# Kernel tuning notes

Measured on AMD Instinct MI355X. Metric: run time of the kernel, lower is better.

The kernel has to match this reference:

```python
import jax, jax.numpy as jnp
import numpy as np

B, N, E, H, F, L, S = 4, 384, 768, 32, 3072, 12, 512
D = E // H


def setup_inputs() -> dict:
    key = jax.random.key(0)
    ks = jax.random.split(key, 32)
    inp = {}
    # forward args
    inp['node_type'] = jax.random.randint(ks[0], (B, N, 1), 1, S + 1)  # table has S+1 rows; 0 = pad (unused)
    inp['node_input_feature'] = jax.random.normal(ks[1], (B, N, E), jnp.float32)
    inp['in_degree'] = jax.random.randint(ks[2], (B, N), 0, S)
    inp['out_degree'] = jax.random.randint(ks[3], (B, N), 0, S)
    inp['attn_bias'] = jax.random.normal(ks[4], (B, N, N), jnp.float32) * 0.1
    inp['spatial_pos'] = jax.random.randint(ks[5], (B, N, N), 0, S)
    # embedding tables (normal stddev 0.02, as in the flax module)
    inp['node_emb'] = jax.random.normal(ks[6], (S + 1, E), jnp.float32) * 0.02
    inp['in_deg_emb'] = jax.random.normal(ks[7], (S, E), jnp.float32) * 0.02
    inp['out_deg_emb'] = jax.random.normal(ks[8], (S, E), jnp.float32) * 0.02
    inp['sp_emb'] = jax.random.normal(ks[9], (S, H), jnp.float32) * 0.02
    inp['sp_emb_rev'] = jax.random.normal(ks[10], (S, H), jnp.float32) * 0.02
    # per-layer weights, stacked along leading L axis
    se, sf = 1.0 / np.sqrt(E), 1.0 / np.sqrt(F)
    inp['Wq'] = jax.random.normal(ks[11], (L, E, E), jnp.float32) * se
    inp['bq'] = jax.random.normal(ks[12], (L, E), jnp.float32) * se
    inp['Wk'] = jax.random.normal(ks[13], (L, E, E), jnp.float32) * se
    inp['bk'] = jax.random.normal(ks[14], (L, E), jnp.float32) * se
    inp['Wv'] = jax.random.normal(ks[15], (L, E, E), jnp.float32) * se
    inp['bv'] = jax.random.normal(ks[16], (L, E), jnp.float32) * se
    inp['Wo'] = jax.random.normal(ks[17], (L, E, E), jnp.float32) * se
    inp['bo'] = jnp.zeros((L, E), jnp.float32)
    inp['W1'] = jax.random.normal(ks[18], (L, E, F), jnp.float32) * se
    inp['b1'] = jax.random.normal(ks[19], (L, F), jnp.float32) * se
    inp['W2'] = jax.random.normal(ks[20], (L, F, E), jnp.float32) * sf
    inp['b2'] = jax.random.normal(ks[21], (L, E), jnp.float32) * sf
    inp['ln1_s'] = jnp.ones((L, E), jnp.float32)
    inp['ln1_b'] = jnp.zeros((L, E), jnp.float32)
    inp['ln2_s'] = jnp.ones((L, E), jnp.float32)
    inp['ln2_b'] = jnp.zeros((L, E), jnp.float32)
    return inp


def _layernorm(x, scale, bias, eps=1e-5):
    m = x.mean(-1, keepdims=True)
    v = ((x - m) ** 2).mean(-1, keepdims=True)
    return (x - m) / jnp.sqrt(v + eps) * scale + bias


def _encoder(node_type, node_input_feature, in_degree, out_degree, attn_bias, spatial_pos,
             node_emb, in_deg_emb, out_deg_emb, sp_emb, sp_emb_rev,
             Wq, bq, Wk, bk, Wv, bv, Wo, bo, W1, b1, W2, b2, ln1_s, ln1_b, ln2_s, ln2_b):
    nt = node_type[..., 0]                               # [B,N]
    padding_mask = nt == 0                               # [B,N]
    # node features: node_emb(node_type).sum(-2) + degree embeddings + input feature
    x = (node_emb[node_type].sum(axis=-2)
         + in_deg_emb[in_degree] + out_deg_emb[out_degree]
         + node_input_feature)                           # [B,N,E]
    # spatial attention bias: [B,N,N,H] -> [B,H,N,N], plus graph-level attn_bias
    sb = sp_emb[spatial_pos] + sp_emb_rev[jnp.transpose(spatial_pos, (0, 2, 1))]
    bias = jnp.transpose(sb, (0, 3, 1, 2)) + attn_bias[:, None]  # [B,H,N,N]

    x = jnp.transpose(x, (1, 0, 2))                      # [N,B,E]
    scaling = D ** (-0.5)
    neg_inf = jnp.float32(-jnp.inf)

    def layer(x, p):
        wq, bq_, wk, bk_, wv, bv_, wo, bo_, w1, b1_, w2, b2_, s1, t1, s2, t2 = p
        q = ((x @ wq) + bq_) * scaling                   # [N,B,E], bias scaled too (faithful)
        k = (x @ wk) + bk_
        v = (x @ wv) + bv_
        q = q.reshape(N, B, H, D)
        k = k.reshape(N, B, H, D)
        v = v.reshape(N, B, H, D)
        w = jnp.einsum('nbhd,mbhd->bhnm', q, k) + bias   # [B,H,N,N]
        w = jnp.where(padding_mask[:, None, None, :], neg_inf, w)
        probs = jax.nn.softmax(w.astype(jnp.float32), axis=-1).astype(x.dtype)
        a = jnp.einsum('bhnm,mbhd->nbhd', probs, v).reshape(N, B, E)
        a = a @ wo + bo_
        x = _layernorm(x + a, s1, t1)                    # post-LN
        h = jax.nn.gelu(x @ w1 + b1_)                    # approximate gelu (flax default)
        h = h @ w2 + b2_
        x = _layernorm(x + h, s2, t2)
        return x, None

    xs = (Wq, bq, Wk, bk, Wv, bv, Wo, bo, W1, b1, W2, b2, ln1_s, ln1_b, ln2_s, ln2_b)
    x, _ = jax.lax.scan(layer, x, xs)
    return x                                             # [N,B,E]


def reference(node_type, node_input_feature, in_degree, out_degree, attn_bias, spatial_pos,
              node_emb, in_deg_emb, out_deg_emb, sp_emb, sp_emb_rev,
              Wq, bq, Wk, bk, Wv, bv, Wo, bo, W1, b1, W2, b2, ln1_s, ln1_b, ln2_s, ln2_b):
    return _encoder(node_type, node_input_feature, in_degree, out_degree, attn_bias, spatial_pos,
                    node_emb, in_deg_emb, out_deg_emb, sp_emb, sp_emb_rev,
                    Wq, bq, Wk, bk, Wv, bv, Wo, bo, W1, b1, W2, b2, ln1_s, ln1_b, ln2_s, ln2_b)
```

## Files before the change

### kernel.cpp

```cpp
#include <hip/hip_runtime.h>
#include <hip/hip_bf16.h>

#define Bb 4
#define Nn 384
#define Ee 768
#define Hh 32
#define Ff 3072
#define Ll 12
#define Ss 512
#define Mm (Nn*Bb)

typedef __attribute__((ext_vector_type(8))) short bf16x8;
typedef __attribute__((ext_vector_type(4))) float f32x4;
typedef unsigned short u16;

__device__ __forceinline__ u16 f2b(float f) {
  union { float f; unsigned int i; } c; c.f = f;
  unsigned int x = c.i;
  return (u16)((x + 0x7fffu + ((x >> 16) & 1u)) >> 16);
}
__device__ __forceinline__ float b2f(u16 u) {
  union { unsigned int i; float f; } c; c.i = ((unsigned int)u) << 16; return c.f;
}
__device__ __forceinline__ unsigned pkcvt(float lo, float hi) {
  unsigned r;
  asm("v_cvt_pk_bf16_f32 %0, %1, %2" : "=v"(r) : "v"(lo), "v"(hi));
  return r;
}
__device__ __forceinline__ void gload_lds16(const void* g, void* l) {
  __builtin_amdgcn_global_load_lds((__attribute__((address_space(1))) void*)(g),
                                   (__attribute__((address_space(3))) void*)(l), 16, 0, 0);
}

__device__ __forceinline__ void embed_body(
    int r, const int* __restrict__ node_type, const float* __restrict__ nif,
    const int* __restrict__ in_deg, const int* __restrict__ out_deg,
    const float* __restrict__ node_emb, const float* __restrict__ ind_emb,
    const float* __restrict__ outd_emb,
    float* __restrict__ x, u16* __restrict__ xb)
{
  const int n = r / Bb, b = r % Bb;
  const int nt  = node_type[b*Nn + n];
  const int idg = in_deg[b*Nn + n];
  const int odg = out_deg[b*Nn + n];
  for (int c = threadIdx.x; c < Ee; c += 256) {
    float val = node_emb[(size_t)nt*Ee + c] + ind_emb[(size_t)idg*Ee + c]
              + outd_emb[(size_t)odg*Ee + c] + nif[((size_t)b*Nn + n)*Ee + c];
    x[(size_t)r*Ee + c] = val;
    xb[(size_t)r*Ee + c] = f2b(val);
  }
}

__device__ __forceinline__ void spT_body(
    int bid, char* smemRaw, const int* __restrict__ sp, int* __restrict__ spT)
{
  int (*tile)[33] = (int(*)[33])smemRaw;
  const int b = bid / 144, rem = bid % 144;
  const int m0 = (rem % 12) * 32, n0 = (rem / 12) * 32;
  const int tx = threadIdx.x & 31, ty = threadIdx.x >> 5;
  for (int i = ty; i < 32; i += 8)
    tile[i][tx] = sp[((size_t)b*Nn + n0 + i)*Nn + m0 + tx];
  __syncthreads();
  for (int i = ty; i < 32; i += 8)
    spT[((size_t)b*Nn + m0 + i)*Nn + n0 + tx] = tile[tx][i];
}

__device__ __forceinline__ void biaspre_body(
    int bid2, char* smemRaw,
    const float* __restrict__ atb, const int* __restrict__ sp, const int* __restrict__ spT,
    const float* __restrict__ sp_emb, const float* __restrict__ sp_emb_rev,
    u16* __restrict__ biasb)
{
  float* spc  = (float*)smemRaw;
  float* sprc = spc + 512;
  const int bx = bid2 % 24, h = (bid2 / 24) % Hh, b = bid2 / (24 * Hh);
  const int t = threadIdx.x;
  for (int i = t; i < 512; i += 256) {
    spc[i]  = sp_emb[(size_t)i*Hh + h];
    sprc[i] = sp_emb_rev[(size_t)i*Hh + h];
  }
  __syncthreads();
  const int qi = t >> 4;
  const int ml = (t & 15) << 2;
  const size_t rowb = ((size_t)b*Nn + bx*16 + qi)*Nn;
  u16* outb = biasb + ((size_t)(b*Hh + h)*24 + bx)*24*256;
  #pragma unroll
  for (int mg = 0; mg < 6; ++mg) {
    const int m = mg*64 + ml;
    float4 a4 = *(const float4*)(atb + rowb + m);
    int4  s4 = *(const int4*)(sp  + rowb + m);
    int4  t4 = *(const int4*)(spT + rowb + m);
    const int tt = m >> 4, hi2 = (m >> 2) & 3;
    uint2 u;
    u.x = pkcvt(a4.x + spc[s4.x] + sprc[t4.x], a4.y + spc[s4.y] + sprc[t4.y]);
    u.y = pkcvt(a4.z + spc[s4.z] + sprc[t4.z], a4.w + spc[s4.w] + sprc[t4.w]);
    *(uint2*)(outb + (tt >> 1)*512 + (hi2*16 + qi)*8 + (tt & 1)*4) = u;
  }
}

__device__ __forceinline__ void wconv_body(
    int tid, int layer, char* smemRaw,
    const float* Wq, const float* Wk, const float* Wv,
    const float* Wo, const float* W1, const float* W2, u16* slot)
{
  float (*tile)[65] = (float(*)[65])smemRaw;
  const float* src; u16* dst; int Ns, Ks;
  if (tid < 432)       { int seg = tid / 144; tid -= seg*144;
                         src = (seg==0?Wq:(seg==1?Wk:Wv)) + (size_t)layer*Ee*Ee;
                         dst = slot + (size_t)seg*589824; Ns = 768; Ks = 768; }
  else if (tid < 576)  { tid -= 432; src = Wo + (size_t)layer*Ee*Ee; dst = slot + 1769472; Ns = 768;  Ks = 768; }
  else if (tid < 1152) { tid -= 576; src = W1 + (size_t)layer*Ee*Ff; dst = slot + 2359296; Ns = 3072; Ks = 768; }
  else                 { tid -= 1152; src = W2 + (size_t)layer*Ff*Ee; dst = slot + 4718592; Ns = 768; Ks = 3072; }
  const int tc = Ns >> 6;
  const int tk = tid / tc, tn = tid % tc;
  const int t = threadIdx.x;
  #pragma unroll
  for (int i = 0; i < 4; ++i) {
    const int id = t + i*256;
    const int r = id >> 4, c = (id & 15) << 2;
    float4 v = *(const float4*)(src + (size_t)(tk*64 + r)*Ns + tn*64 + c);
    tile[r][c+0] = v.x; tile[r][c+1] = v.y; tile[r][c+2] = v.z; tile[r][c+3] = v.w;
  }
  __syncthreads();
  #pragma unroll
  for (int i = 0; i < 2; ++i) {
    const int ch = t + i*256;
    const int n = ch >> 3, kc = (ch & 7) << 3;
    uint4 u;
    u.x = pkcvt(tile[kc+0][n], tile[kc+1][n]);
    u.y = pkcvt(tile[kc+2][n], tile[kc+3][n]);
    u.z = pkcvt(tile[kc+4][n], tile[kc+5][n]);
    u.w = pkcvt(tile[kc+6][n], tile[kc+7][n]);
    *(uint4*)(dst + (size_t)(tn*64 + n)*Ks + tk*64 + kc) = u;
  }
}

__global__ __launch_bounds__(256) void wconv_kernel(
    const float* __restrict__ Wq, const float* __restrict__ Wk, const float* __restrict__ Wv,
    const float* __restrict__ Wo, const float* __restrict__ W1, const float* __restrict__ W2,
    int layer, u16* __restrict__ slot)
{
  __shared__ __align__(16) char smem[16640];
  wconv_body(blockIdx.x, layer, smem, Wq, Wk, Wv, Wo, W1, W2, slot);
}

__global__ __launch_bounds__(256) void prep_kernel(
    const int* __restrict__ node_type, const float* __restrict__ nif,
    const int* __restrict__ in_deg, const int* __restrict__ out_deg,
    const float* __restrict__ node_emb, const float* __restrict__ ind_emb,
    const float* __restrict__ outd_emb,
    float* __restrict__ x, u16* __restrict__ xb,
    const int* __restrict__ sp, int* __restrict__ spT,
    const float* __restrict__ Wq, const float* __restrict__ Wk, const float* __restrict__ Wv,
    const float* __restrict__ Wo, const float* __restrict__ W1, const float* __restrict__ W2,
    u16* __restrict__ slot0)
{
  __shared__ __align__(16) char smem[16640];
  const int bid = blockIdx.x;
  if (bid < 1536) {
    embed_body(bid, node_type, nif, in_deg, out_deg, node_emb, ind_emb, outd_emb, x, xb);
  } else if (bid < 2112) {
    spT_body(bid - 1536, smem, sp, spT);
  } else {
    wconv_body(bid - 2112, 0, smem, Wq, Wk, Wv, Wo, W1, W2, slot0);
  }
}

template<int EPI>
__device__ __forceinline__ void gemm_body(
    char* smemRaw, int bx0, int by0, int gx, int nwg, int zz,
    const u16* __restrict__ A, const u16* __restrict__ Bw,
    const float* __restrict__ b0, const float* __restrict__ b1, const float* __restrict__ b2,
    int Kfull, int Kc, float scaleQ,
    float* __restrict__ outF, u16* __restrict__ outB)
{
  u16 (*As)[128][64] = (u16(*)[128][64])smemRaw;
  u16 (*Bs)[64][64]  = (u16(*)[64][64])(smemRaw + 32768);
  const int t = threadIdx.x, lane = t & 63, wave = t >> 6;
  int bx = bx0, by = by0;
  {
    const int bid = bx + gx * by;
    const int cpx = nwg >> 3;
    const int s = (bid & 7) * cpx + (bid >> 3);
    bx = s % gx; by = s / gx;
  }
  const int m0 = bx * 128, n0 = by * 64;
  const int k0 = zz * Kc;
  const int wm = wave >> 1, wn = wave & 1;
  const int ql = lane & 15, hi = lane >> 4;
  const int nk = Kc >> 6;
  const int sr = t >> 3;
  const int sslot = (t & 7) ^ (sr & 7);
  const size_t aoff = (size_t)(m0 + sr)*Kfull + k0 + (sslot << 3);
  const size_t boff = (size_t)(n0 + sr)*Kfull + k0 + (sslot << 3);
  const size_t rstep = (size_t)32 * Kfull;

  int aro[4][2], bro[2][2];
  #pragma unroll
  for (int ks = 0; ks < 2; ++ks) {
    const int kb = (((ks<<2) + hi) ^ (ql & 7)) << 4;
    #pragma unroll
    for (int f = 0; f < 4; ++f) aro[f][ks] = (wm*64 + f*16 + ql)*128 + kb;
    #pragma unroll
    for (int f = 0; f < 2; ++f) bro[f][ks] = (wn*32 + f*16 + ql)*128 + kb;
  }

  f32x4 acc[4][2];
  #pragma unroll
  for (int a = 0; a < 4; ++a)
    #pragma unroll
    for (int c = 0; c < 2; ++c) acc[a][c] = (f32x4){0.f,0.f,0.f,0.f};

  #pragma unroll
  for (int i = 0; i < 4; ++i)
    gload_lds16(A + aoff + i*rstep, (char*)&As[0][0][0] + i*4096 + t*16);
  #pragma unroll
  for (int i = 0; i < 2; ++i)
    gload_lds16(Bw + boff + i*rstep, (char*)&Bs[0][0][0] + i*4096 + t*16);

  for (int kt = 0; kt < nk; ++kt) {
    const int cur = kt & 1, nxt = cur ^ 1;
    const bool pre = (kt + 1 < nk);
    if (pre) {
      const size_t kk = (size_t)(kt + 1) << 6;
      #pragma unroll
      for (int i = 0; i < 4; ++i)
        gload_lds16(A + aoff + kk + i*rstep, (char*)&As[nxt][0][0] + i*4096 + t*16);
      #pragma unroll
      for (int i = 0; i < 2; ++i)
        gload_lds16(Bw + boff + kk + i*rstep, (char*)&Bs[nxt][0][0] + i*4096 + t*16);
      asm volatile("s_waitcnt vmcnt(6)" ::: "memory");
    } else {
      asm volatile("s_waitcnt vmcnt(0)" ::: "memory");
    }
    __builtin_amdgcn_s_barrier();
    __builtin_amdgcn_sched_barrier(0);

    const char* aBase = (const char*)&As[cur][0][0];
    const char* bBase = (const char*)&Bs[cur][0][0];
    bf16x8 af[4][2], bf[2][2];
    #pragma unroll
    for (int f = 0; f < 4; ++f)
      #pragma unroll
      for (int ks = 0; ks < 2; ++ks)
        af[f][ks] = *(const bf16x8*)(aBase + aro[f][ks]);
    #pragma unroll
    for (int f = 0; f < 2; ++f)
      #pragma unroll
      for (int ks = 0; ks < 2; ++ks)
        bf[f][ks] = *(const bf16x8*)(bBase + bro[f][ks]);
    #pragma unroll
    for (int ks = 0; ks < 2; ++ks)
      #pragma unroll
      for (int fm = 0; fm < 4; ++fm)
        #pragma unroll
        for (int fn = 0; fn < 2; ++fn)
          acc[fm][fn] = __builtin_amdgcn_mfma_f32_16x16x32_bf16(af[fm][ks], bf[fn][ks], acc[fm][fn], 0, 0, 0);
    if (pre) {
      __builtin_amdgcn_sched_barrier(0);
      __builtin_amdgcn_s_barrier();
    }
  }

  #pragma unroll
  for (int fm = 0; fm < 4; ++fm) {
    const int rowb = m0 + wm*64 + fm*16 + hi*4;
    #pragma unroll
    for (int fn = 0; fn < 2; ++fn) {
      const int gcol = n0 + wn*32 + fn*16 + ql;
      float bv, scale = 1.0f;
      if (EPI == 0) {
        const int seg = gcol / 768;
        const int cw = gcol - seg*768;
        bv = (seg == 0) ? b0[cw] : ((seg == 1) ? b1[cw] : b2[cw]);
        if (seg == 0) scale = scaleQ;
      } else if (EPI == 1) {
        bv = (zz == 0) ? b0[gcol] : 0.0f;
      } else {
        bv = b0[gcol];
      }
      f32x4 v = acc[fm][fn];
      #pragma unroll
      for (int j = 0; j < 4; ++j) {
        float val = (v[j] + bv) * scale;
        if (EPI == 0) {
          outB[(size_t)(rowb + j) * 2304 + gcol] = f2b(val);
        } else if (EPI == 1) {
          outF[(size_t)zz * (Mm*768) + (size_t)(rowb + j) * 768 + gcol] = val;
        } else {
          float arg = 0.7978845608028654f * (val + 0.044715f * val * val * val);
          float e = __expf(2.0f * arg);
          float g = 0.5f * val * (2.0f - 2.0f / (e + 1.0f));
          outB[(size_t)(rowb + j) * 3072 + gcol] = f2b(g);
        }
      }
    }
  }
}

template<int EPI>
__global__ __launch_bounds__(256) void gemm3_kernel(
    const u16* __restrict__ A, const u16* __restrict__ Bw,
    const float* __restrict__ b0, const float* __restrict__ b1, const float* __restrict__ b2,
    int Kfull, int Kc, float scaleQ,
    float* __restrict__ outF, u16* __restrict__ outB)
{
  __shared__ __align__(16) char smem[49152];
  gemm_body<EPI>(smem, blockIdx.x, blockIdx.y, gridDim.x, gridDim.x*gridDim.y,
                 blockIdx.z, A, Bw, b0, b1, b2, Kfull, Kc, scaleQ, outF, outB);
}

__global__ __launch_bounds__(256) void qkv0b_kernel(
    const u16* __restrict__ A, const u16* __restrict__ qkvT,
    const float* __restrict__ b0, const float* __restrict__ b1, const float* __restrict__ b2,
    float scaleQ, u16* __restrict__ outB,
    const float* __restrict__ atb, const int* __restrict__ sp, const int* __restrict__ spT,
    const float* __restrict__ sp_emb, const float* __restrict__ sp_emb_rev,
    u16* __restrict__ biasb)
{
  __shared__ __align__(16) char smem[49152];
  const int bid = blockIdx.x;
  if (bid < 432) {
    gemm_body<0>(smem, bid % 12, bid / 12, 12, 432, 0,
                 A, qkvT, b0, b1, b2, 768, 768, scaleQ, nullptr, outB);
  } else {
    biaspre_body(bid - 432, smem, atb, sp, spT, sp_emb, sp_emb_rev, biasb);
  }
}

__global__ __launch_bounds__(256) void ffn2w_kernel(
    const u16* __restrict__ A, const u16* __restrict__ w2T,
    const float* __restrict__ b2v, float* __restrict__ outF,
    const float* __restrict__ Wq, const float* __restrict__ Wk, const float* __restrict__ Wv,
    const float* __restrict__ Wo, const float* __restrict__ W1, const float* __restrict__ W2,
    int layerNext, u16* __restrict__ slotNext, int doW)
{
  __shared__ __align__(16) char smem[49152];
  const int bid = blockIdx.x;
  if (bid < 576) {
    const int zz = bid / 144, r = bid - zz*144;
    gemm_body<1>(smem, r % 12, r / 12, 12, 144, zz,
                 A, w2T, b2v, b2v, b2v, 3072, 768, 1.0f, outF, nullptr);
  } else if (doW) {
    wconv_body(bid - 576, layerNext, smem, Wq, Wk, Wv, Wo, W1, W2, slotNext);
  }
}

template<int PREBIAS>
__global__ __launch_bounds__(256) void attn2_kernel(
    const u16* __restrict__ qkv,
    const u16* __restrict__ biasb,
    const float* __restrict__ atb, const int* __restrict__ sp, const int* __restrict__ spT,
    const float* __restrict__ sp_emb, const float* __restrict__ sp_emb_rev,
    u16* __restrict__ ab)
{
  __shared__ __align__(16) u16 Kt[384][32];
  __shared__ __align__(16) u16 Vt[32][392];
  __shared__ __align__(16) u16 Qt[128][32];
  __shared__ __align__(16) u16 Pw[4][16][32];
  __shared__ float spc[512], sprc[512];
  const int bid = blockIdx.x;
  const int pair = bid % 3;
  const int h = (bid / 3) % Hh;
  const int b = bid / (3 * Hh);
  const int t = threadIdx.x, lane = t & 63, wave = t >> 6;
  const int ql = lane & 15, hi = lane >> 4;

  for (int idx = t; idx < 384*3; idx += 256) {
    const int m = idx / 3, c = idx - m*3;
    const u16* base = qkv + ((size_t)m*Bb + b)*2304 + h*24 + c*8;
    uint4 kk = *(const uint4*)(base + 768);
    uint4 vv = *(const uint4*)(base + 1536);
    *(uint4*)&Kt[m][c*8] = kk;
    Vt[c*8+0][m] = (u16)(vv.x & 0xffffu); Vt[c*8+1][m] = (u16)(vv.x >> 16);
    Vt[c*8+2][m] = (u16)(vv.y & 0xffffu); Vt[c*8+3][m] = (u16)(vv.y >> 16);
    Vt[c*8+4][m] = (u16)(vv.z & 0xffffu); Vt[c*8+5][m] = (u16)(vv.z >> 16);
    Vt[c*8+6][m] = (u16)(vv.w & 0xffffu); Vt[c*8+7][m] = (u16)(vv.w >> 16);
  }
  for (int idx = t; idx < 384*2; idx += 256)
    *(uint2*)&Kt[idx>>1][24 + (idx&1)*4] = make_uint2(0u, 0u);
  for (int idx = t; idx < 8*196; idx += 256)
    *(unsigned*)((char*)&Vt[24][0] + idx*4) = 0u;
  for (int idx = t; idx < 128*3; idx += 256) {
    const int qr = idx / 3, c = idx - qr*3;
    const u16* base = qkv + ((size_t)(pair*128 + qr)*Bb + b)*2304 + h*24 + c*8;
    *(uint4*)&Qt[qr][c*8] = *(const uint4*)base;
  }
  for (int idx = t; idx < 128*2; idx += 256)
    *(uint2*)&Qt[idx>>1][24 + (idx&1)*4] = make_uint2(0u, 0u);
  if (!PREBIAS) {
    for (int i = t; i < 512; i += 256) {
      spc[i]  = sp_emb[(size_t)i*Hh + h];
      sprc[i] = sp_emb_rev[(size_t)i*Hh + h];
    }
  }
  __syncthreads();

  for (int qi = 0; qi < 2; ++qi) {
    const int ntile = pair*2 + qi;
    const int q0 = ntile*64 + wave*16;
    const int q = q0 + ql;
    const bf16x8 qf = *(const bf16x8*)&Qt[qi*64 + wave*16 + ql][hi*8];

    f32x4 f[24];
    const size_t crow = ((size_t)b*Nn + q)*Nn;
    if (PREBIAS) {
      const u16* bp = biasb + (((size_t)(b*Hh + h)*24 + ntile*4 + wave)*24)*256 + lane*8;
      #pragma unroll
      for (int tt2 = 0; tt2 < 12; ++tt2) {
        uint4 bb = *(const uint4*)(bp + tt2*512);
        {
          bf16x8 kf = *(const bf16x8*)&Kt[(2*tt2)*16 + ql][hi*8];
          f32x4 z = (f32x4){0.f,0.f,0.f,0.f};
          f32x4 s = __builtin_amdgcn_mfma_f32_16x16x32_bf16(kf, qf, z, 0, 0, 0);
          s[0] += b2f((u16)(bb.x & 0xffffu)); s[1] += b2f((u16)(bb.x >> 16));
          s[2] += b2f((u16)(bb.y & 0xffffu)); s[3] += b2f((u16)(bb.y >> 16));
          f[2*tt2] = s;
        }
        {
          bf16x8 kf = *(const bf16x8*)&Kt[(2*tt2+1)*16 + ql][hi*8];
          f32x4 z = (f32x4){0.f,0.f,0.f,0.f};
          f32x4 s = __builtin_amdgcn_mfma_f32_16x16x32_bf16(kf, qf, z, 0, 0, 0);
          s[0] += b2f((u16)(bb.z & 0xffffu)); s[1] += b2f((u16)(bb.z >> 16));
          s[2] += b2f((u16)(bb.w & 0xffffu)); s[3] += b2f((u16)(bb.w >> 16));
          f[2*tt2+1] = s;
        }
      }
    } else {
      #pragma unroll
      for (int tt = 0; tt < 24; ++tt) {
        bf16x8 kf = *(const bf16x8*)&Kt[tt*16 + ql][hi*8];
        f32x4 z = (f32x4){0.f,0.f,0.f,0.f};
        f32x4 s = __builtin_amdgcn_mfma_f32_16x16x32_bf16(kf, qf, z, 0, 0, 0);
        const int off = tt*16 + hi*4;
        int4 s4 = *(const int4*)(sp + crow + off);
        int4 t4 = *(const int4*)(spT + crow + off);
        float4 a4 = *(const float4*)(atb + crow + off);
        s[0] += a4.x + spc[s4.x] + sprc[t4.x];
        s[1] += a4.y + spc[s4.y] + sprc[t4.y];
        s[2] += a4.z + spc[s4.z] + sprc[t4.z];
        s[3] += a4.w + spc[s4.w] + sprc[t4.w];
        f[tt] = s;
      }
    }

    float mx = -3.0e38f;
    #pragma unroll
    for (int tt = 0; tt < 24; ++tt)
      mx = fmaxf(mx, fmaxf(fmaxf(f[tt][0], f[tt][1]), fmaxf(f[tt][2], f[tt][3])));
    mx = fmaxf(mx, __shfl_xor(mx, 16, 64));
    mx = fmaxf(mx, __shfl_xor(mx, 32, 64));
    float sum = 0.f;
    #pragma unroll
    for (int tt = 0; tt < 24; ++tt) {
      #pragma unroll
      for (int j = 0; j < 4; ++j) { f[tt][j] = __expf(f[tt][j] - mx); sum += f[tt][j]; }
    }
    sum += __shfl_xor(sum, 16, 64);
    sum += __shfl_xor(sum, 32, 64);
    const float inv = 1.0f / sum;

    f32x4 o0 = (f32x4){0.f,0.f,0.f,0.f}, o1 = (f32x4){0.f,0.f,0.f,0.f};
    char* prow = (char*)&Pw[wave][ql][0];
    const int swz = (ql & 3) << 4;
    #pragma unroll
    for (int c = 0; c < 12; ++c) {
      unsigned w0 = pkcvt(f[2*c][0],   f[2*c][1]);
      unsigned w1 = pkcvt(f[2*c][2],   f[2*c][3]);
      unsigned w2 = pkcvt(f[2*c+1][0], f[2*c+1][1]);
      unsigned w3 = pkcvt(f[2*c+1][2], f[2*c+1][3]);
      *(unsigned*)(prow + (((hi*8)      ) ^ swz)) = w0;
      *(unsigned*)(prow + (((hi*8) +  4) ^ swz)) = w1;
      *(unsigned*)(prow + (((hi*8) + 32) ^ swz)) = w2;
      *(unsigned*)(prow + (((hi*8) + 36) ^ swz)) = w3;
      bf16x8 a = *(const bf16x8*)(prow + ((hi*16) ^ swz));
      bf16x8 v0 = *(const bf16x8*)&Vt[ql][c*32 + hi*8];
      bf16x8 v1 = *(const bf16x8*)&Vt[16 + ql][c*32 + hi*8];
      o0 = __builtin_amdgcn_mfma_f32_16x16x32_bf16(a, v0, o0, 0, 0, 0);
      o1 = __builtin_amdgcn_mfma_f32_16x16x32_bf16(a, v1, o1, 0, 0, 0);
    }

    #pragma unroll
    for (int j = 0; j < 4; ++j) {
      float invj = __shfl(inv, hi*4 + j, 64);
      const int qg = q0 + hi*4 + j;
      u16* orow = ab + ((size_t)qg*Bb + b)*Ee + h*24;
      orow[ql] = f2b(o0[j] * invj);
      if (ql < 8) orow[16 + ql] = f2b(o1[j] * invj);
    }
  }
}

template<int NP>
__global__ __launch_bounds__(256) void ln_kernel(
    const float* __restrict__ xin, const float* __restrict__ delta,
    const float* __restrict__ gamma, const float* __restrict__ beta,
    float* __restrict__ xout, u16* __restrict__ xb)
{
  const int wave = threadIdx.x >> 6, lane = threadIdx.x & 63;
  const int r = blockIdx.x * 4 + wave;
  const size_t base = (size_t)r * Ee;
  const int c0 = lane * 12;
  float v[12];
  #pragma unroll
  for (int i = 0; i < 3; ++i) {
    float4 xv = *(const float4*)(xin + base + c0 + i*4);
    v[i*4+0] = xv.x; v[i*4+1] = xv.y; v[i*4+2] = xv.z; v[i*4+3] = xv.w;
  }
  #pragma unroll
  for (int p = 0; p < NP; ++p) {
    const float* dp = delta + (size_t)p*(Mm*768) + base + c0;
    #pragma unroll
    for (int i = 0; i < 3; ++i) {
      float4 dv = *(const float4*)(dp + i*4);
      v[i*4+0] += dv.x; v[i*4+1] += dv.y; v[i*4+2] += dv.z; v[i*4+3] += dv.w;
    }
  }
  float s = 0.f;
  #pragma unroll
  for (int i = 0; i < 12; ++i) s += v[i];
  #pragma unroll
  for (int off = 1; off < 64; off <<= 1) s += __shfl_xor(s, off, 64);
  const float mean = s * (1.0f / 768.0f);
  float qs = 0.f;
  #pragma unroll
  for (int i = 0; i < 12; ++i) { float d = v[i] - mean; qs += d * d; }
  #pragma unroll
  for (int off = 1; off < 64; off <<= 1) qs += __shfl_xor(qs, off, 64);
  const float rstd = rsqrtf(qs * (1.0f / 768.0f) + 1e-5f);
  float o[12];
  #pragma unroll
  for (int i = 0; i < 3; ++i) {
    float4 g4 = *(const float4*)(gamma + c0 + i*4);
    float4 b4 = *(const float4*)(beta + c0 + i*4);
    o[i*4+0] = (v[i*4+0] - mean) * rstd * g4.x + b4.x;
    o[i*4+1] = (v[i*4+1] - mean) * rstd * g4.y + b4.y;
    o[i*4+2] = (v[i*4+2] - mean) * rstd * g4.z + b4.z;
    o[i*4+3] = (v[i*4+3] - mean) * rstd * g4.w + b4.w;
    *(float4*)(xout + base + c0 + i*4) = make_float4(o[i*4+0], o[i*4+1], o[i*4+2], o[i*4+3]);
  }
  #pragma unroll
  for (int i = 0; i < 3; ++i) {
    uint2 u;
    u.x = pkcvt(o[i*4+0], o[i*4+1]);
    u.y = pkcvt(o[i*4+2], o[i*4+3]);
    *(uint2*)(xb + base + c0 + i*4) = u;
  }
}

extern "C" void kernel_launch(void* const* d_in, const int* in_sizes, int n_in,
                              void* d_out, int out_size, void* d_ws, size_t ws_size,
                              hipStream_t stream) {
  const int*   node_type  = (const int*)d_in[0];
  const float* nif        = (const float*)d_in[1];
  const int*   in_deg     = (const int*)d_in[2];
  const int*   out_deg    = (const int*)d_in[3];
  const float* atb        = (const float*)d_in[4];
  const int*   sp         = (const int*)d_in[5];
  const float* node_emb   = (const float*)d_in[6];
  const float* ind_emb    = (const float*)d_in[7];
  const float* outd_emb   = (const float*)d_in[8];
  const float* sp_emb     = (const float*)d_in[9];
  const float* sp_emb_rev = (const float*)d_in[10];
  const float* Wq = (const float*)d_in[11]; const float* bq = (const float*)d_in[12];
  const float* Wk = (const float*)d_in[13]; const float* bk = (const float*)d_in[14];
  const float* Wv = (const float*)d_in[15]; const float* bv = (const float*)d_in[16];
  const float* Wo = (const float*)d_in[17]; const float* bo = (const float*)d_in[18];
  const float* W1 = (const float*)d_in[19]; const float* b1 = (const float*)d_in[20];
  const float* W2 = (const float*)d_in[21]; const float* b2 = (const float*)d_in[22];
  const float* ln1s = (const float*)d_in[23]; const float* ln1b = (const float*)d_in[24];
  const float* ln2s = (const float*)d_in[25]; const float* ln2b = (const float*)d_in[26];

  char* ws = (char*)d_ws;
  float* x      = (float*)(ws);
  u16*   xb     = (u16*)(ws +  4718592);
  u16*   qkvb16 = (u16*)(ws +  7077888);
  u16*   abuf   = (u16*)(ws + 14155776);
  u16*   hb     = (u16*)(ws + 16515072);
  float* obufP  = (float*)(ws + 25952256);
  int*   spTb   = (int*)(ws + 44826624);
  u16*   biasb  = (u16*)(ws + 47185920);
  u16*   wTs0   = (u16*)(ws + 84934656);
  u16*   wTs1   = (u16*)(ws + 99090432);
  const bool useBias = ws_size >= 113246208ull;
  u16* slots[2] = { wTs0, wTs1 };

  prep_kernel<<<3840, 256, 0, stream>>>(node_type, nif, in_deg, out_deg,
                                        node_emb, ind_emb, outd_emb, x, xb,
                                        sp, spTb,
                                        Wq, Wk, Wv, Wo, W1, W2, slots[0]);

  const float scaleQ = 0.2041241452319315f;

  for (int l = 0; l < Ll; ++l) {
    const float *bql = bq + (size_t)l*Ee, *bkl = bk + (size_t)l*Ee, *bvl = bv + (size_t)l*Ee;
    const float *bol = bo + (size_t)l*Ee;
    const float *b1l = b1 + (size_t)l*Ff, *b2l = b2 + (size_t)l*Ee;

    u16* slot = slots[l & 1];
    u16* slotN = slots[(l + 1) & 1];
    const u16* qkvT = slot;
    const u16* woT  = slot + 1769472;
    const u16* w1T  = slot + 2359296;
    const u16* w2T  = slot + 4718592;

    if (l == 0 && useBias)
      qkv0b_kernel<<<3504, 256, 0, stream>>>(xb, qkvT, bql, bkl, bvl, scaleQ, qkvb16,
                                             atb, sp, spTb, sp_emb, sp_emb_rev, biasb);
    else
      gemm3_kernel<0><<<dim3(12, 36), 256, 0, stream>>>(xb, qkvT, bql, bkl, bvl,
                                                        768, 768, scaleQ, nullptr, qkvb16);
    if (useBias)
      attn2_kernel<1><<<384, 256, 0, stream>>>(qkvb16, biasb, atb, sp, spTb,
                                               sp_emb, sp_emb_rev, abuf);
    else
      attn2_kernel<0><<<384, 256, 0, stream>>>(qkvb16, nullptr, atb, sp, spTb,
                                               sp_emb, sp_emb_rev, abuf);
    gemm3_kernel<1><<<dim3(12, 12, 2), 256, 0, stream>>>(abuf, woT, bol, bol, bol,
                                                         768, 384, 1.0f, obufP, nullptr);
    ln_kernel<2><<<Mm/4, 256, 0, stream>>>(x, obufP, ln1s + (size_t)l*Ee, ln1b + (size_t)l*Ee, x, xb);
    gemm3_kernel<2><<<dim3(12, 48), 256, 0, stream>>>(xb, w1T, b1l, b1l, b1l,
                                                      768, 768, 1.0f, nullptr, hb);
    ffn2w_kernel<<<2304, 256, 0, stream>>>(hb, w2T, b2l, obufP,
                                           Wq, Wk, Wv, Wo, W1, W2,
                                           l + 1, slotN, (l + 1 < Ll) ? 1 : 0);
    float* xdst = (l == Ll - 1) ? (float*)d_out : x;
    ln_kernel<4><<<Mm/4, 256, 0, stream>>>(x, obufP, ln2s + (size_t)l*Ee, ln2b + (size_t)l*Ee, xdst, xb);
  }
}
```

Baseline: 1.174 ms.

## Fuse output-projection GEMM and LayerNorm into one launch with a global counter

Merges the Wo split-K GEMM and the following residual+LayerNorm into a single kernel. GEMM blocks increment a per-layer atomic counter after a threadfence, and LN blocks spin-wait until all 288 GEMM blocks finish. This removes one kernel launch and its gap per layer. In exchange, LN blocks that are resident early occupy CUs while spinning, and progress depends on all GEMM blocks being scheduled before the waiting blocks starve them. It also needs a memset of the counters and a slightly larger workspace.

```diff
diff --git a/kernel.cpp b/kernel.cpp
--- a/kernel.cpp
+++ b/kernel.cpp
@@ -308,6 +308,99 @@
   __shared__ __align__(16) char smem[49152];
   gemm_body<EPI>(smem, blockIdx.x, blockIdx.y, gridDim.x, gridDim.x*gridDim.y,
                  blockIdx.z, A, Bw, b0, b1, b2, Kfull, Kc, scaleQ, outF, outB);
+}
+
+template<int NP>
+__device__ __forceinline__ void ln_body(
+    int rb, const float* __restrict__ xin, const float* __restrict__ delta,
+    const float* __restrict__ gamma, const float* __restrict__ beta,
+    float* __restrict__ xout, u16* __restrict__ xb)
+{
+  const int wave = threadIdx.x >> 6, lane = threadIdx.x & 63;
+  const int r = rb * 4 + wave;
+  const size_t base = (size_t)r * Ee;
+  const int c0 = lane * 12;
+  float v[12];
+  #pragma unroll
+  for (int i = 0; i < 3; ++i) {
+    float4 xv = *(const float4*)(xin + base + c0 + i*4);
+    v[i*4+0] = xv.x; v[i*4+1] = xv.y; v[i*4+2] = xv.z; v[i*4+3] = xv.w;
+  }
+  #pragma unroll
+  for (int p = 0; p < NP; ++p) {
+    const float* dp = delta + (size_t)p*(Mm*768) + base + c0;
+    #pragma unroll
+    for (int i = 0; i < 3; ++i) {
+      float4 dv = *(const float4*)(dp + i*4);
+      v[i*4+0] += dv.x; v[i*4+1] += dv.y; v[i*4+2] += dv.z; v[i*4+3] += dv.w;
+    }
+  }
+  float s = 0.f;
+  #pragma unroll
+  for (int i = 0; i < 12; ++i) s += v[i];
+  #pragma unroll
+  for (int off = 1; off < 64; off <<= 1) s += __shfl_xor(s, off, 64);
+  const float mean = s * (1.0f / 768.0f);
+  float qs = 0.f;
+  #pragma unroll
+  for (int i = 0; i < 12; ++i) { float d = v[i] - mean; qs += d * d; }
+  #pragma unroll
+  for (int off = 1; off < 64; off <<= 1) qs += __shfl_xor(qs, off, 64);
+  const float rstd = rsqrtf(qs * (1.0f / 768.0f) + 1e-5f);
+  float o[12];
+  #pragma unroll
+  for (int i = 0; i < 3; ++i) {
+    float4 g4 = *(const float4*)(gamma + c0 + i*4);
+    float4 b4 = *(const float4*)(beta + c0 + i*4);
+    o[i*4+0] = (v[i*4+0] - mean) * rstd * g4.x + b4.x;
+    o[i*4+1] = (v[i*4+1] - mean) * rstd * g4.y + b4.y;
+    o[i*4+2] = (v[i*4+2] - mean) * rstd * g4.z + b4.z;
+    o[i*4+3] = (v[i*4+3] - mean) * rstd * g4.w + b4.w;
+    *(float4*)(xout + base + c0 + i*4) = make_float4(o[i*4+0], o[i*4+1], o[i*4+2], o[i*4+3]);
+  }
+  #pragma unroll
+  for (int i = 0; i < 3; ++i) {
+    uint2 u;
+    u.x = pkcvt(o[i*4+0], o[i*4+1]);
+    u.y = pkcvt(o[i*4+2], o[i*4+3]);
+    *(uint2*)(xb + base + c0 + i*4) = u;
+  }
+}
+
+template<int NP>
+__global__ __launch_bounds__(256) void ln_kernel(
+    const float* __restrict__ xin, const float* __restrict__ delta,
+    const float* __restrict__ gamma, const float* __restrict__ beta,
+    float* __restrict__ xout, u16* __restrict__ xb)
+{
+  ln_body<NP>(blockIdx.x, xin, delta, gamma, beta, xout, xb);
+}
+
+__global__ __launch_bounds__(256) void oln_kernel(
+    const u16* __restrict__ A, const u16* __restrict__ woT, const float* __restrict__ bol,
+    float* __restrict__ obufP,
+    const float* __restrict__ xin, const float* __restrict__ gamma,
+    const float* __restrict__ beta,
+    float* __restrict__ xout, u16* __restrict__ xb,
+    unsigned* __restrict__ ctr)
+{
+  __shared__ __align__(16) char smem[49152];
+  const int bid = blockIdx.x;
+  if (bid < 288) {
+    const int zz = bid / 144, r = bid - zz*144;
+    gemm_body<1>(smem, r % 12, r / 12, 12, 144, zz,
+                 A, woT, bol, bol, bol, 768, 384, 1.0f, obufP, nullptr);
+    __threadfence();
+    __syncthreads();
+    if (threadIdx.x == 0) atomicAdd(ctr, 1u);
+  } else {
+    if (threadIdx.x == 0) {
+      while (atomicAdd(ctr, 0u) < 288u) __builtin_amdgcn_s_sleep(8);
+    }
+    __syncthreads();
+    __threadfence();
+    ln_body<2>(bid - 288, xin, obufP, gamma, beta, xout, xb);
+  }
 }
 
 __global__ __launch_bounds__(256) void qkv0b_kernel(
@@ -488,63 +581,6 @@
       orow[ql] = f2b(o0[j] * invj);
       if (ql < 8) orow[16 + ql] = f2b(o1[j] * invj);
     }
-  }
-}
-
-template<int NP>
-__global__ __launch_bounds__(256) void ln_kernel(
-    const float* __restrict__ xin, const float* __restrict__ delta,
-    const float* __restrict__ gamma, const float* __restrict__ beta,
-    float* __restrict__ xout, u16* __restrict__ xb)
-{
-  const int wave = threadIdx.x >> 6, lane = threadIdx.x & 63;
-  const int r = blockIdx.x * 4 + wave;
-  const size_t base = (size_t)r * Ee;
-  const int c0 = lane * 12;
-  float v[12];
-  #pragma unroll
-  for (int i = 0; i < 3; ++i) {
-    float4 xv = *(const float4*)(xin + base + c0 + i*4);
-    v[i*4+0] = xv.x; v[i*4+1] = xv.y; v[i*4+2] = xv.z; v[i*4+3] = xv.w;
-  }
-  #pragma unroll
-  for (int p = 0; p < NP; ++p) {
-    const float* dp = delta + (size_t)p*(Mm*768) + base + c0;
-    #pragma unroll
-    for (int i = 0; i < 3; ++i) {
-      float4 dv = *(const float4*)(dp + i*4);
-      v[i*4+0] += dv.x; v[i*4+1] += dv.y; v[i*4+2] += dv.z; v[i*4+3] += dv.w;
-    }
-  }
-  float s = 0.f;
-  #pragma unroll
-  for (int i = 0; i < 12; ++i) s += v[i];
-  #pragma unroll
-  for (int off = 1; off < 64; off <<= 1) s += __shfl_xor(s, off, 64);
-  const float mean = s * (1.0f / 768.0f);
-  float qs = 0.f;
-  #pragma unroll
-  for (int i = 0; i < 12; ++i) { float d = v[i] - mean; qs += d * d; }
-  #pragma unroll
-  for (int off = 1; off < 64; off <<= 1) qs += __shfl_xor(qs, off, 64);
-  const float rstd = rsqrtf(qs * (1.0f / 768.0f) + 1e-5f);
-  float o[12];
-  #pragma unroll
-  for (int i = 0; i < 3; ++i) {
-    float4 g4 = *(const float4*)(gamma + c0 + i*4);
-    float4 b4 = *(const float4*)(beta + c0 + i*4);
-    o[i*4+0] = (v[i*4+0] - mean) * rstd * g4.x + b4.x;
-    o[i*4+1] = (v[i*4+1] - mean) * rstd * g4.y + b4.y;
-    o[i*4+2] = (v[i*4+2] - mean) * rstd * g4.z + b4.z;
-    o[i*4+3] = (v[i*4+3] - mean) * rstd * g4.w + b4.w;
-    *(float4*)(xout + base + c0 + i*4) = make_float4(o[i*4+0], o[i*4+1], o[i*4+2], o[i*4+3]);
-  }
-  #pragma unroll
-  for (int i = 0; i < 3; ++i) {
-    uint2 u;
-    u.x = pkcvt(o[i*4+0], o[i*4+1]);
-    u.y = pkcvt(o[i*4+2], o[i*4+3]);
-    *(uint2*)(xb + base + c0 + i*4) = u;
   }
 }
 
@@ -582,8 +618,11 @@
   u16*   biasb  = (u16*)(ws + 47185920);
   u16*   wTs0   = (u16*)(ws + 84934656);
   u16*   wTs1   = (u16*)(ws + 99090432);
-  const bool useBias = ws_size >= 113246208ull;
+  unsigned* ctrs = (unsigned*)(ws + 113246208);
+  const bool useBias = ws_size >= 113246464ull;
   u16* slots[2] = { wTs0, wTs1 };
+
+  hipMemsetAsync(ctrs, 0, 12 * sizeof(unsigned), stream);
 
   prep_kernel<<<3840, 256, 0, stream>>>(node_type, nif, in_deg, out_deg,
                                         node_emb, ind_emb, outd_emb, x, xb,
@@ -616,9 +655,15 @@
     else
       attn2_kernel<0><<<384, 256, 0, stream>>>(qkvb16, nullptr, atb, sp, spTb,
                                                sp_emb, sp_emb_rev, abuf);
-    gemm3_kernel<1><<<dim3(12, 12, 2), 256, 0, stream>>>(abuf, woT, bol, bol, bol,
-                                                         768, 384, 1.0f, obufP, nullptr);
-    ln_kernel<2><<<Mm/4, 256, 0, stream>>>(x, obufP, ln1s + (size_t)l*Ee, ln1b + (size_t)l*Ee, x, xb);
+    if (useBias) {
+      oln_kernel<<<672, 256, 0, stream>>>(abuf, woT, bol, obufP,
+                                          x, ln1s + (size_t)l*Ee, ln1b + (size_t)l*Ee,
+                                          x, xb, ctrs + l);
+    } else {
+      gemm3_kernel<1><<<dim3(12, 12, 2), 256, 0, stream>>>(abuf, woT, bol, bol, bol,
+                                                           768, 384, 1.0f, obufP, nullptr);
+      ln_kernel<2><<<Mm/4, 256, 0, stream>>>(x, obufP, ln1s + (size_t)l*Ee, ln1b + (size_t)l*Ee, x, xb);
+    }
     gemm3_kernel<2><<<dim3(12, 48), 256, 0, stream>>>(xb, w1T, b1l, b1l, b1l,
                                                       768, 768, 1.0f, nullptr, hb);
     ffn2w_kernel<<<2304, 256, 0, stream>>>(hb, w2T, b2l, obufP,
```

New measurement: 2.152 ms. 83.3% more time.
